# Kernel tuning notes

Measured on AMD Instinct MI355X. Metric: run time of the kernel, lower is better.

The kernel has to match this reference:

```python
import jax, jax.numpy as jnp
import numpy as np

C = 64  # RDN out_dim

def _make_coord_1d(n):
    r = 1.0 / n
    return -1.0 + r + 2.0 * r * jnp.arange(n, dtype=jnp.float32)

def _unfold3x3(feat):
    # torch F.unfold(feat, 3, padding=1) -> [B, C*9, H, W], ordering c*9 + (ki*3+kj)
    B, Cc, H, W = feat.shape
    p = jnp.pad(feat, ((0, 0), (0, 0), (1, 1), (1, 1)))
    patches = jnp.stack([p[:, :, di:di + H, dj:dj + W]
                         for di in range(3) for dj in range(3)], axis=2)
    return patches.reshape(B, Cc * 9, H, W)

def setup_inputs() -> dict:
    key = jax.random.key(0)
    ks = jax.random.split(key, 5)
    feat = jax.random.normal(ks[0], (1, C, 64, 64), dtype=jnp.float32)
    w1 = jax.random.normal(ks[1], (3, 256), dtype=jnp.float32) * 0.1
    b1 = jax.random.normal(ks[2], (256,), dtype=jnp.float32) * 0.01
    w2 = jax.random.normal(ks[3], (256, C * 9 * 3), dtype=jnp.float32) * 0.02
    b2 = jax.random.normal(ks[4], (C * 9 * 3,), dtype=jnp.float32) * 0.01
    return {"feat": feat, "w1": w1, "b1": b1, "w2": w2, "b2": b2,
            "out_h": 256, "out_w": 256}

def reference(feat, w1, b1, w2, b2, out_h, out_w):
    B, Cc, H, W = feat.shape
    C9 = Cc * 9
    # HR query coords at grid centers, flattened: [q, 2] (dim0 -> H axis)
    cy = _make_coord_1d(out_h)
    cx = _make_coord_1d(out_w)
    coord = jnp.stack(jnp.meshgrid(cy, cx, indexing='ij'), axis=-1).reshape(-1, 2)
    coord = jnp.broadcast_to(coord[None], (B, out_h * out_w, 2))  # [B, q, 2]
    cell = jnp.stack([jnp.full((out_h * out_w,), 2.0 / out_h, jnp.float32),
                      jnp.full((out_h * out_w,), 2.0 / out_w, jnp.float32)], axis=-1)
    cell = jnp.broadcast_to(cell[None], (B, out_h * out_w, 2))

    featu = _unfold3x3(feat)  # [B, C*9, H, W]

    # coord_ = coord - cell/2, clamped query coords
    coord_ = coord - cell * 0.5
    eps = 1e-6
    coord_q = jnp.clip(coord_ + eps, -1.0 + eps, 1.0 - eps)

    # grid_sample nearest, align_corners=False: idx = round(((c+1)*N - 1)/2)
    iy = jnp.clip(jnp.round(((coord_q[..., 0] + 1.0) * H - 1.0) * 0.5), 0, H - 1).astype(jnp.int32)
    ix = jnp.clip(jnp.round(((coord_q[..., 1] + 1.0) * W - 1.0) * 0.5), 0, W - 1).astype(jnp.int32)

    # gather unfolded features at nearest LR cells -> [B, q, C*9]
    q_feat = jax.vmap(lambda f, y, x: f[:, y, x])(featu, iy, ix)  # [B, C9, q]
    q_feat = jnp.swapaxes(q_feat, 1, 2)

    # feat_coord (shifted by half a cell) at gathered indices = -1 + 2*i/N
    q_coord0 = -1.0 + 2.0 * iy.astype(jnp.float32) / H
    q_coord1 = -1.0 + 2.0 * ix.astype(jnp.float32) / W

    rel0 = (coord_[..., 0] - q_coord0) * (H * 0.5)
    rel1 = (coord_[..., 1] - q_coord1) * (W * 0.5)
    r_rev = cell[..., 0] * (H * 0.5)
    mlp_in = jnp.stack([rel0, rel1, r_rev], axis=-1)  # [B, q, 3]

    h = jax.nn.relu(jnp.einsum('bqi,ih->bqh', mlp_in, w1) + b1)
    pred_w = (jnp.einsum('bqh,ho->bqo', h, w2) + b2).reshape(B, -1, C9, 3)

    # per-query 1xC9 @ C9x3 bmm
    rgb = jnp.einsum('bqc,bqco->bqo', q_feat, pred_w)  # [B, q, 3]
    return rgb.reshape(B, out_h, out_w, 3).transpose(0, 3, 1, 2)
```

## Files before the change

### kernel.cpp

```cpp
#include <hip/hip_runtime.h>


#define NOUT 1728

typedef short bf16x8 __attribute__((ext_vector_type(8)));
typedef float f32x4  __attribute__((ext_vector_type(4)));

__device__ inline unsigned short bf16r(float a) {
    const unsigned ua = __builtin_bit_cast(unsigned, a);
    return (unsigned short)((ua + 0x7FFFu + ((ua >> 16) & 1u)) >> 16);
}
__device__ inline unsigned bf16pack(float a, float b) {
    unsigned ua = __builtin_bit_cast(unsigned, a);
    unsigned ub = __builtin_bit_cast(unsigned, b);
    ua = (ua + 0x7FFFu + ((ua >> 16) & 1u)) >> 16;
    ub = (ub + 0x7FFFu + ((ub >> 16) & 1u)) >> 16;
    return ua | (ub << 16);
}

__global__ __launch_bounds__(256, 2) void k_predw(
    const float* __restrict__ w1, const float* __restrict__ b1,
    const float* __restrict__ w2, const float* __restrict__ b2,
    unsigned short* __restrict__ predw16)
{
    __shared__ float h4[4][256];
    __shared__ float red[1024];

    const int tid   = threadIdx.x;
    const int sg    = blockIdx.x / 27;
    const int chunk = blockIdx.x - sg * 27;
    const int o_l   = tid & 63;
    const int q     = tid >> 6;
    const int o     = chunk * 64 + o_l;

    {
        const float wa = w1[tid];
        const float wb = w1[256 + tid];
        const float wc = w1[512 + tid];
        const float bb = b1[tid];
        #pragma unroll
        for (int si = 0; si < 4; ++si) {
            const int s = (sg << 2) + si;
            const float rel0 = (float)(s >> 2) * 0.25f;
            const float rel1 = (float)(s & 3) * 0.25f;
            h4[si][tid] = fmaxf(fmaf(wa, rel0, fmaf(wb, rel1,
                                fmaf(wc, 0.25f, bb))), 0.0f);
        }
    }
    __syncthreads();

    const float* w2c = w2 + (q << 6) * NOUT + o;
    const float* hq0 = &h4[0][q << 6];
    const float* hq1 = &h4[1][q << 6];
    const float* hq2 = &h4[2][q << 6];
    const float* hq3 = &h4[3][q << 6];

    float a0 = 0.f, a1 = 0.f, a2 = 0.f, a3 = 0.f;
    #pragma unroll 16
    for (int j = 0; j < 64; ++j) {
        const float v = w2c[j * NOUT];
        a0 = fmaf(hq0[j], v, a0);
        a1 = fmaf(hq1[j], v, a1);
        a2 = fmaf(hq2[j], v, a2);
        a3 = fmaf(hq3[j], v, a3);
    }

    *(float4*)&red[tid << 2] = make_float4(a0, a1, a2, a3);
    __syncthreads();

    {
        const int ol = tid >> 2;
        const int si = tid & 3;
        const int oo = chunk * 64 + ol;
        float a = red[(0 * 64 + ol) * 4 + si] + red[(1 * 64 + ol) * 4 + si]
                + red[(2 * 64 + ol) * 4 + si] + red[(3 * 64 + ol) * 4 + si]
                + b2[oo];
        const int ct = oo / 3;
        const int k  = oo - ct * 3;
        const int c  = (ct * 7282) >> 16;
        const int tp = ct - c * 9;
        const int m  = ((sg << 2) + si) * 3 + k;
        predw16[m * 576 + tp * 64 + c] = bf16r(a);
    }
}

__global__ __launch_bounds__(256, 1) void k_conv(
    const float* __restrict__ feat, const unsigned short* __restrict__ predw16,
    float* __restrict__ out)
{
    __shared__ f32x4 red[3 * 64];

    const int tid  = threadIdx.x;
    const int lane = tid & 63;
    const int w    = tid >> 6;
    const int bid  = blockIdx.x;
    const int mt   = bid >> 8;
    const int nt   = bid & 255;
    const int y0   = nt >> 2;
    const int x0   = (nt & 3) << 4;

    const int lc = lane & 15;
    const int lk = lane >> 4;

    int xadr[3]; float xmsk[3];
    #pragma unroll
    for (int d = 0; d < 3; ++d) {
        const int rx = x0 + lc + d - 1;
        xmsk[d] = ((unsigned)rx < 64u) ? 1.0f : 0.0f;
        xadr[d] = rx < 0 ? 0 : (rx > 63 ? 63 : rx);
    }
    int yadr[3]; float ymsk[3];
    #pragma unroll
    for (int d = 0; d < 3; ++d) {
        const int ry = y0 + d - 1;
        ymsk[d] = ((unsigned)ry < 64u) ? 1.0f : 0.0f;
        yadr[d] = (ry < 0 ? 0 : (ry > 63 ? 63 : ry)) << 6;
    }

    const unsigned short* arow = predw16 + (mt * 16 + lc) * 576 + (lk << 3);

    f32x4 acc = {0.0f, 0.0f, 0.0f, 0.0f};

    #pragma unroll
    for (int i = 0; i < 5; ++i) {
        const int kk  = w + (i << 2);
        const int kkc = kk > 17 ? 17 : kk;
        const float vld = (kk < 18) ? 1.0f : 0.0f;
        const int tap = kkc >> 1;
        const int dr  = (tap >= 6) ? 2 : (tap >= 3 ? 1 : 0);
        const int dc  = tap - dr * 3;
        const int c0  = ((kkc & 1) << 5) + (lk << 3);
        const float* fb = feat + (c0 << 12) + yadr[dr] + xadr[dc];
        const float  mk = ymsk[dr] * xmsk[dc] * vld;

        const float v0 = fb[0]       * mk;
        const float v1 = fb[1 << 12] * mk;
        const float v2 = fb[2 << 12] * mk;
        const float v3 = fb[3 << 12] * mk;
        const float v4 = fb[4 << 12] * mk;
        const float v5 = fb[5 << 12] * mk;
        const float v6 = fb[6 << 12] * mk;
        const float v7 = fb[7 << 12] * mk;

        uint4 bb;
        bb.x = bf16pack(v0, v1);
        bb.y = bf16pack(v2, v3);
        bb.z = bf16pack(v4, v5);
        bb.w = bf16pack(v6, v7);
        const bf16x8 bfrag = __builtin_bit_cast(bf16x8, bb);
        const bf16x8 afrag = *(const bf16x8*)(arow + 32 * kkc);

        acc = __builtin_amdgcn_mfma_f32_16x16x32_bf16(afrag, bfrag, acc,
                                                      0, 0, 0);
    }

    if (w > 0) red[(w - 1) * 64 + lane] = acc;
    __syncthreads();

    if (w == 0) {
        #pragma unroll
        for (int q = 0; q < 3; ++q) {
            const f32x4 v = red[q * 64 + lane];
            acc[0] += v[0]; acc[1] += v[1]; acc[2] += v[2]; acc[3] += v[3];
        }
        #pragma unroll
        for (int r = 0; r < 4; ++r) {
            const int m = mt * 16 + (lk << 2) + r;
            const int s = (m * 171) >> 9;
            const int k = m - s * 3;
            const int y = (y0 << 2) + (s >> 2);
            const int x = ((x0 + lc) << 2) + (s & 3);
            out[k * 65536 + y * 256 + x] = acc[r];
        }
    }
}

extern "C" void kernel_launch(void* const* d_in, const int* in_sizes, int n_in,
                              void* d_out, int out_size, void* d_ws, size_t ws_size,
                              hipStream_t stream) {
    const float* feat = (const float*)d_in[0];
    const float* w1   = (const float*)d_in[1];
    const float* b1   = (const float*)d_in[2];
    const float* w2   = (const float*)d_in[3];
    const float* b2   = (const float*)d_in[4];
    float* out = (float*)d_out;
    unsigned short* predw16 = (unsigned short*)d_ws;

    hipLaunchKernelGGL(k_predw, dim3(108), dim3(256), 0, stream,
                       w1, b1, w2, b2, predw16);
    hipLaunchKernelGGL(k_conv, dim3(768), dim3(256), 0, stream,
                       feat, predw16, out);
}
```

Before: 14.62 us.

## Fuse predw and conv kernels into one launch with atomic flag handoff

Merges the two kernels into a single 768-block launch. The first 108 blocks compute the bf16 pred weights and then raise a global counter with release semantics. Every block gathers its feature fragments before spin-waiting on the counter, then runs the MFMA stage. The aim is to remove the second launch and the gap between kernels, and to overlap the feature loads with the weight computation. In exchange it adds a memset launch, a spin-wait that relies on all producer blocks being resident, and a remapped block-to-tile order.

```diff
diff --git a/kernel.cpp b/kernel.cpp
--- a/kernel.cpp
+++ b/kernel.cpp
@@ -18,86 +18,90 @@
     return ua | (ub << 16);
 }
 
-__global__ __launch_bounds__(256, 2) void k_predw(
-    const float* __restrict__ w1, const float* __restrict__ b1,
-    const float* __restrict__ w2, const float* __restrict__ b2,
-    unsigned short* __restrict__ predw16)
+__global__ __launch_bounds__(256, 1) void k_all(
+    const float* __restrict__ feat, const float* __restrict__ w1,
+    const float* __restrict__ b1,   const float* __restrict__ w2,
+    const float* __restrict__ b2,   unsigned short* predw16,
+    unsigned* flag, float* __restrict__ out)
 {
     __shared__ float h4[4][256];
-    __shared__ float red[1024];
-
-    const int tid   = threadIdx.x;
-    const int sg    = blockIdx.x / 27;
-    const int chunk = blockIdx.x - sg * 27;
-    const int o_l   = tid & 63;
-    const int q     = tid >> 6;
-    const int o     = chunk * 64 + o_l;
-
-    {
-        const float wa = w1[tid];
-        const float wb = w1[256 + tid];
-        const float wc = w1[512 + tid];
-        const float bb = b1[tid];
-        #pragma unroll
-        for (int si = 0; si < 4; ++si) {
-            const int s = (sg << 2) + si;
-            const float rel0 = (float)(s >> 2) * 0.25f;
-            const float rel1 = (float)(s & 3) * 0.25f;
-            h4[si][tid] = fmaxf(fmaf(wa, rel0, fmaf(wb, rel1,
-                                fmaf(wc, 0.25f, bb))), 0.0f);
-        }
-    }
-    __syncthreads();
-
-    const float* w2c = w2 + (q << 6) * NOUT + o;
-    const float* hq0 = &h4[0][q << 6];
-    const float* hq1 = &h4[1][q << 6];
-    const float* hq2 = &h4[2][q << 6];
-    const float* hq3 = &h4[3][q << 6];
-
-    float a0 = 0.f, a1 = 0.f, a2 = 0.f, a3 = 0.f;
-    #pragma unroll 16
-    for (int j = 0; j < 64; ++j) {
-        const float v = w2c[j * NOUT];
-        a0 = fmaf(hq0[j], v, a0);
-        a1 = fmaf(hq1[j], v, a1);
-        a2 = fmaf(hq2[j], v, a2);
-        a3 = fmaf(hq3[j], v, a3);
-    }
-
-    *(float4*)&red[tid << 2] = make_float4(a0, a1, a2, a3);
-    __syncthreads();
-
-    {
-        const int ol = tid >> 2;
-        const int si = tid & 3;
-        const int oo = chunk * 64 + ol;
-        float a = red[(0 * 64 + ol) * 4 + si] + red[(1 * 64 + ol) * 4 + si]
-                + red[(2 * 64 + ol) * 4 + si] + red[(3 * 64 + ol) * 4 + si]
-                + b2[oo];
-        const int ct = oo / 3;
-        const int k  = oo - ct * 3;
-        const int c  = (ct * 7282) >> 16;
-        const int tp = ct - c * 9;
-        const int m  = ((sg << 2) + si) * 3 + k;
-        predw16[m * 576 + tp * 64 + c] = bf16r(a);
-    }
-}
-
-__global__ __launch_bounds__(256, 1) void k_conv(
-    const float* __restrict__ feat, const unsigned short* __restrict__ predw16,
-    float* __restrict__ out)
-{
-    __shared__ f32x4 red[3 * 64];
-
-    const int tid  = threadIdx.x;
+    __shared__ float redA[1024];
+    __shared__ f32x4 redB[192];
+
+    const int tid = threadIdx.x;
+    const int bid = blockIdx.x;
+
+    if (bid < 108) {
+        const int sg    = bid / 27;
+        const int chunk = bid - sg * 27;
+        const int o_l   = tid & 63;
+        const int q     = tid >> 6;
+        const int o     = chunk * 64 + o_l;
+
+        {
+            const float wa = w1[tid];
+            const float wb = w1[256 + tid];
+            const float wc = w1[512 + tid];
+            const float bb = b1[tid];
+            #pragma unroll
+            for (int si = 0; si < 4; ++si) {
+                h4[si][tid] = fmaxf(
+                    fmaf(wa, (float)sg * 0.25f,
+                    fmaf(wb, (float)si * 0.25f,
+                    fmaf(wc, 0.25f, bb))), 0.0f);
+            }
+        }
+        __syncthreads();
+
+        const float* w2c = w2 + (q << 6) * NOUT + o;
+        const float* hq0 = &h4[0][q << 6];
+        const float* hq1 = &h4[1][q << 6];
+        const float* hq2 = &h4[2][q << 6];
+        const float* hq3 = &h4[3][q << 6];
+
+        float a0 = 0.f, a1 = 0.f, a2 = 0.f, a3 = 0.f;
+        #pragma unroll 16
+        for (int j = 0; j < 64; ++j) {
+            const float v = w2c[j * NOUT];
+            a0 = fmaf(hq0[j], v, a0);
+            a1 = fmaf(hq1[j], v, a1);
+            a2 = fmaf(hq2[j], v, a2);
+            a3 = fmaf(hq3[j], v, a3);
+        }
+        *(float4*)&redA[tid << 2] = make_float4(a0, a1, a2, a3);
+        __syncthreads();
+
+        {
+            const int ol = tid >> 2;
+            const int si = tid & 3;
+            const int oo = chunk * 64 + ol;
+            float a = redA[(0 * 64 + ol) * 4 + si]
+                    + redA[(1 * 64 + ol) * 4 + si]
+                    + redA[(2 * 64 + ol) * 4 + si]
+                    + redA[(3 * 64 + ol) * 4 + si] + b2[oo];
+            const int ct = oo / 3;
+            const int k  = oo - ct * 3;
+            const int c  = (ct * 7282) >> 16;
+            const int tp = ct - c * 9;
+            const int m  = ((sg << 2) + si) * 3 + k;
+            predw16[m * 576 + tp * 64 + c] = bf16r(a);
+        }
+        __syncthreads();
+        if (tid == 0) {
+            __builtin_amdgcn_fence(__ATOMIC_RELEASE, "agent");
+            __hip_atomic_fetch_add(flag, 1u, __ATOMIC_RELEASE,
+                                   __HIP_MEMORY_SCOPE_AGENT);
+        }
+    }
+
     const int lane = tid & 63;
-    const int w    = tid >> 6;
-    const int bid  = blockIdx.x;
-    const int mt   = bid >> 8;
-    const int nt   = bid & 255;
-    const int y0   = nt >> 2;
-    const int x0   = (nt & 3) << 4;
+    const int wv   = tid >> 6;
+    const int sx   = bid & 7;
+    const int u    = bid >> 3;
+    const int mt   = u >> 5;
+    const int v    = u & 31;
+    const int y0   = (sx << 3) | (v >> 2);
+    const int x0   = (v & 3) << 4;
 
     const int lc = lane & 15;
     const int lk = lane >> 4;
@@ -117,13 +121,10 @@
         yadr[d] = (ry < 0 ? 0 : (ry > 63 ? 63 : ry)) << 6;
     }
 
-    const unsigned short* arow = predw16 + (mt * 16 + lc) * 576 + (lk << 3);
-
-    f32x4 acc = {0.0f, 0.0f, 0.0f, 0.0f};
-
+    bf16x8 bfr[5];
     #pragma unroll
     for (int i = 0; i < 5; ++i) {
-        const int kk  = w + (i << 2);
+        const int kk  = wv + (i << 2);
         const int kkc = kk > 17 ? 17 : kk;
         const float vld = (kk < 18) ? 1.0f : 0.0f;
         const int tap = kkc >> 1;
@@ -147,21 +148,37 @@
         bb.y = bf16pack(v2, v3);
         bb.z = bf16pack(v4, v5);
         bb.w = bf16pack(v6, v7);
-        const bf16x8 bfrag = __builtin_bit_cast(bf16x8, bb);
+        bfr[i] = __builtin_bit_cast(bf16x8, bb);
+    }
+
+    if (tid == 0) {
+        while (__hip_atomic_load(flag, __ATOMIC_RELAXED,
+                                 __HIP_MEMORY_SCOPE_AGENT) < 108u)
+            __builtin_amdgcn_s_sleep(8);
+    }
+    __syncthreads();
+    __builtin_amdgcn_fence(__ATOMIC_ACQUIRE, "agent");
+
+    const unsigned short* arow = predw16 + (mt * 16 + lc) * 576 + (lk << 3);
+
+    f32x4 acc = {0.0f, 0.0f, 0.0f, 0.0f};
+    #pragma unroll
+    for (int i = 0; i < 5; ++i) {
+        const int kk  = wv + (i << 2);
+        const int kkc = kk > 17 ? 17 : kk;
         const bf16x8 afrag = *(const bf16x8*)(arow + 32 * kkc);
-
-        acc = __builtin_amdgcn_mfma_f32_16x16x32_bf16(afrag, bfrag, acc,
+        acc = __builtin_amdgcn_mfma_f32_16x16x32_bf16(afrag, bfr[i], acc,
                                                       0, 0, 0);
     }
 
-    if (w > 0) red[(w - 1) * 64 + lane] = acc;
+    if (wv > 0) redB[(wv - 1) * 64 + lane] = acc;
     __syncthreads();
 
-    if (w == 0) {
+    if (wv == 0) {
         #pragma unroll
         for (int q = 0; q < 3; ++q) {
-            const f32x4 v = red[q * 64 + lane];
-            acc[0] += v[0]; acc[1] += v[1]; acc[2] += v[2]; acc[3] += v[3];
+            const f32x4 pv = redB[q * 64 + lane];
+            acc[0] += pv[0]; acc[1] += pv[1]; acc[2] += pv[2]; acc[3] += pv[3];
         }
         #pragma unroll
         for (int r = 0; r < 4; ++r) {
@@ -184,10 +201,11 @@
     const float* w2   = (const float*)d_in[3];
     const float* b2   = (const float*)d_in[4];
     float* out = (float*)d_out;
+
     unsigned short* predw16 = (unsigned short*)d_ws;
-
-    hipLaunchKernelGGL(k_predw, dim3(108), dim3(256), 0, stream,
-                       w1, b1, w2, b2, predw16);
-    hipLaunchKernelGGL(k_conv, dim3(768), dim3(256), 0, stream,
-                       feat, predw16, out);
-}
+    unsigned* flag = (unsigned*)((char*)d_ws + 55296);
+
+    hipMemsetAsync(flag, 0, 4, stream);
+    hipLaunchKernelGGL(k_all, dim3(768), dim3(256), 0, stream,
+                       feat, w1, b1, w2, b2, predw16, flag, out);
+}
```

New measurement: 55.51 us. 280% more time.
